# Optimization experiments

Hardware: AMD Instinct MI355X
Metric: run time of the kernel (lower is better)

Reference implementation:

```python
import jax, jax.numpy as jnp
import numpy as np

EPS = 1e-5

def layer_norm(x, w, b):
    # Faithful to the module: divides by (sqrt(var) + eps), NOT sqrt(var + eps).
    m = jnp.mean(x, axis=-1, keepdims=True)
    v = jnp.mean((x - m) ** 2, axis=-1, keepdims=True)
    return (x - m) / (jnp.sqrt(v) + EPS) * w + b

def setup_inputs() -> dict:
    key = jax.random.key(0)
    B, S, E, H, F = 8, 2048, 512, 8, 2048
    ks = jax.random.split(key, 8)
    def lin(k, fin, fout):
        k1, k2 = jax.random.split(k)
        return (jax.random.normal(k1, (fin, fout), jnp.float32) * (1.0 / np.sqrt(fin)),
                jax.random.normal(k2, (fout,), jnp.float32) * 0.01)
    WQ, bQ = lin(ks[0], E, E)
    WK, bK = lin(ks[1], E, E)
    WV, bV = lin(ks[2], E, E)
    WY, bY = lin(ks[3], E, E)
    W1, b1 = lin(ks[4], E, F)
    W2, b2 = lin(ks[5], F, E)
    x = jax.random.normal(ks[6], (B, S, E), jnp.float32)
    return {
        "x": x,
        "WQ": WQ, "bQ": bQ, "WK": WK, "bK": bK, "WV": WV, "bV": bV,
        "WY": WY, "bY": bY,
        "ln1_w": jnp.ones((E,), jnp.float32), "ln1_b": jnp.zeros((E,), jnp.float32),
        "W1": W1, "b1": b1, "W2": W2, "b2": b2,
        "ln2_w": jnp.ones((E,), jnp.float32), "ln2_b": jnp.zeros((E,), jnp.float32),
    }

def attention(x, WQ, bQ, WK, bK, WV, bV, WY, bY, num_heads=8):
    B, S, E = x.shape
    D = E // num_heads  # head_size
    def split(t):  # (B,S,E) -> (B,H,S,D)
        return t.reshape(B, S, num_heads, D).transpose(0, 2, 1, 3)
    q = split(x @ WQ + bQ)
    k = split(x @ WK + bK)
    v = split(x @ WV + bV)
    scores = jnp.einsum('bhsd,bhtd->bhst', q, k) / jnp.sqrt(jnp.float32(D))
    w = jax.nn.softmax(scores, axis=-1)  # full (B,H,S,S) attention matrix, as in original
    y = jnp.einsum('bhst,bhtd->bhsd', w, v)
    y = y.transpose(0, 2, 1, 3).reshape(B, S, E)  # merge heads
    return y @ WY + bY

def reference(x, WQ, bQ, WK, bK, WV, bV, WY, bY, ln1_w, ln1_b, W1, b1, W2, b2, ln2_w, ln2_b):
    attn_out = attention(x, WQ, bQ, WK, bK, WV, bV, WY, bY)
    h = layer_norm(x + attn_out, ln1_w, ln1_b)  # post-norm
    mlp = jax.nn.gelu(h @ W1 + b1, approximate=False) @ W2 + b2
    out = layer_norm(h + mlp, ln2_w, ln2_b)
    return out
```

## Files before the change

kernel.cpp:

```cpp
#include <hip/hip_runtime.h>
#include <hip/hip_bf16.h>
#include <cstdint>

typedef unsigned short u16;
typedef __bf16 __attribute__((ext_vector_type(8))) bf16x8;
typedef float __attribute__((ext_vector_type(4))) f32x4;
typedef float __attribute__((ext_vector_type(16))) f32x16;

#define B_ 8
#define S_ 2048
#define E_ 512
#define H_ 8
#define D_ 64
#define F_ 2048
#define MTOT (B_ * S_)
#define QSCALE 0.18033688011112042f
#define MFIX 12.0f

static __device__ __forceinline__ float bf2f(u16 u) {
    union { uint32_t i; float f; } x;
    x.i = ((uint32_t)u) << 16;
    return x.f;
}
static __device__ __forceinline__ u16 f2bf(float f) {
    __hip_bfloat16 h = __float2bfloat16(f);
    return *reinterpret_cast<u16*>(&h);
}
static __device__ __forceinline__ float fast_exp2(float x) {
    float r;
    asm("v_exp_f32 %0, %1" : "=v"(r) : "v"(x));
    return r;
}
static __device__ __forceinline__ float fast_exp2_neg(float x) {
    float r;
    asm("v_exp_f32 %0, -%1" : "=v"(r) : "v"(x));
    return r;
}
static __device__ __forceinline__ float fast_rcp(float x) {
    float r;
    asm("v_rcp_f32 %0, %1" : "=v"(r) : "v"(x));
    return r;
}
static __device__ __forceinline__ uint32_t cvt_pk_bf16(float a, float b) {
    uint32_t r;
    asm("v_cvt_pk_bf16_f32 %0, %1, %2" : "=v"(r) : "v"(a), "v"(b));
    return r;
}
static __device__ __forceinline__ float fast_gelu(float v) {
    float x2 = v * v;
    float w = v * fmaf(0.10294818f, x2, 2.3022066f);
    float e = fast_exp2_neg(w);
    return v * fast_rcp(1.0f + e);
}

__global__ __launch_bounds__(256) void prep(const float* __restrict__ x,
                                            u16* __restrict__ xb,
                                            const float* __restrict__ WQ,
                                            const float* __restrict__ WK,
                                            const float* __restrict__ WV,
                                            const float* __restrict__ WY,
                                            const float* __restrict__ W1,
                                            const float* __restrict__ W2,
                                            u16* __restrict__ WQKVT,
                                            u16* __restrict__ WYT,
                                            u16* __restrict__ W1T,
                                            u16* __restrict__ W2T,
                                            const float* __restrict__ bQ,
                                            const float* __restrict__ bK,
                                            const float* __restrict__ bV,
                                            float* __restrict__ bqkv) {
    const int bid = blockIdx.x;
    const int tid = threadIdx.x;
    if (bid < 4096) {
        int i = bid * 256 + tid;
        const float4* p = reinterpret_cast<const float4*>(x) + (size_t)i * 2;
        float4 a = p[0], b = p[1];
        uint4 o;
        o.x = cvt_pk_bf16(a.x, a.y);
        o.y = cvt_pk_bf16(a.z, a.w);
        o.z = cvt_pk_bf16(b.x, b.y);
        o.w = cvt_pk_bf16(b.z, b.w);
        *reinterpret_cast<uint4*>(xb + (size_t)i * 8) = o;
        return;
    }
    int r = bid - 4096;
    if (r >= 3072) {
        int i = (r - 3072) * 256 + tid;
        if (i < 1536) bqkv[i] = i < 512 ? bQ[i] : (i < 1024 ? bK[i - 512] : bV[i - 1024]);
        return;
    }
    __shared__ float tile[32][33];
    const float* src;
    u16* dst;
    int K, N, bx, by;
    if (r < 1024) {
        int w = r >> 8, idx = r & 255;
        bx = idx & 15; by = idx >> 4; K = 512; N = 512;
        src = w == 0 ? WQ : (w == 1 ? WK : (w == 2 ? WV : WY));
        dst = (w == 3) ? WYT : (WQKVT + (size_t)w * 512 * 512);
    } else if (r < 2048) {
        int idx = r - 1024;
        bx = idx & 63; by = idx >> 6; K = 512; N = 2048;
        src = W1; dst = W1T;
    } else {
        int idx = r - 2048;
        bx = idx & 15; by = idx >> 4; K = 2048; N = 512;
        src = W2; dst = W2T;
    }
    const int tx = tid & 31, ty = tid >> 5;
    int n0 = bx * 32, k0 = by * 32;
    for (int i = ty; i < 32; i += 8)
        tile[i][tx] = src[(size_t)(k0 + i) * N + n0 + tx];
    __syncthreads();
    for (int i = ty; i < 32; i += 8)
        dst[(size_t)(n0 + i) * K + k0 + tx] = f2bf(tile[tx][i]);
}

template <int ACT, int SPLIT>
__global__ __launch_bounds__(512) void gemm_bt(const u16* __restrict__ A,
                                               const u16* __restrict__ BT,
                                               const float* __restrict__ bias,
                                               void* __restrict__ Cv,
                                               u16* __restrict__ Vtg,
                                               int Mdim, int Ndim, int Kdim) {
    __shared__ u16 As[128 * 64];
    __shared__ u16 Bs[128 * 64];
    const int tid = threadIdx.x;
    const int wave = tid >> 6, lane = tid & 63;
    const int lr = lane & 15, lg = lane >> 4;

    const int gx = gridDim.x;
    int lin = blockIdx.y * gx + blockIdx.x;
    const int nwg = gx * gridDim.y;
    if ((nwg & 7) == 0) {
        int cpx = nwg >> 3;
        lin = (lin & 7) * cpx + (lin >> 3);
    }
    const int m0 = (lin / gx) * 128, n0 = (lin % gx) * 128;
    const int wrow = (wave >> 2) * 64, wcol = (wave & 3) * 32;

    f32x4 acc[4][2];
#pragma unroll
    for (int i = 0; i < 4; i++)
#pragma unroll
        for (int j = 0; j < 2; j++) acc[i][j] = (f32x4){0.f, 0.f, 0.f, 0.f};

    const int stagerow = tid >> 3;
    const int stagechunk = (tid & 7) * 8;

    for (int k0 = 0; k0 < Kdim; k0 += 64) {
        __syncthreads();
#pragma unroll
        for (int it = 0; it < 2; ++it) {
            int row = stagerow + it * 64;
            const u16* ga = A + (size_t)(m0 + row) * Kdim + k0 + stagechunk;
            const u16* gb = BT + (size_t)(n0 + row) * Kdim + k0 + stagechunk;
            __builtin_amdgcn_global_load_lds(
                (const __attribute__((address_space(1))) void*)ga,
                (__attribute__((address_space(3))) void*)(As + row * 64 + stagechunk),
                16, 0, 0);
            __builtin_amdgcn_global_load_lds(
                (const __attribute__((address_space(1))) void*)gb,
                (__attribute__((address_space(3))) void*)(Bs + row * 64 + stagechunk),
                16, 0, 0);
        }
        __syncthreads();
#pragma unroll
        for (int kk = 0; kk < 64; kk += 32) {
            bf16x8 af[4], bfr[2];
#pragma unroll
            for (int i = 0; i < 4; i++)
                af[i] = *reinterpret_cast<const bf16x8*>(As + (wrow + i * 16 + lr) * 64 + kk + lg * 8);
#pragma unroll
            for (int j = 0; j < 2; j++)
                bfr[j] = *reinterpret_cast<const bf16x8*>(Bs + (wcol + j * 16 + lr) * 64 + kk + lg * 8);
#pragma unroll
            for (int i = 0; i < 4; i++)
#pragma unroll
                for (int j = 0; j < 2; j++)
                    acc[i][j] = __builtin_amdgcn_mfma_f32_16x16x32_bf16(af[i], bfr[j], acc[i][j], 0, 0, 0);
        }
    }

#pragma unroll
    for (int j = 0; j < 2; j++) {
        int col = n0 + wcol + j * 16 + lr;
        float bv = bias[col];
        int seg = col >> 9, c2 = col & 511;
#pragma unroll
        for (int i = 0; i < 4; i++) {
            int rowb = m0 + wrow + i * 16 + lg * 4;
            float vv[4];
#pragma unroll
            for (int r = 0; r < 4; r++) {
                float v = acc[i][j][r] + bv;
                if (ACT == 1) v = fast_gelu(v);
                if (SPLIT) { if (seg == 0) v *= QSCALE; }
                vv[r] = v;
            }
            uint32_t p01 = cvt_pk_bf16(vv[0], vv[1]);
            uint32_t p23 = cvt_pk_bf16(vv[2], vv[3]);
            if (SPLIT) {
                if (seg == 2) {
                    int bb = rowb >> 11, s = rowb & 2047;
                    *reinterpret_cast<uint2*>(Vtg + ((size_t)bb * E_ + c2) * S_ + s) =
                        (uint2){p01, p23};
                } else {
                    u16* dst = (u16*)Cv + (size_t)seg * ((size_t)MTOT * 512) + (size_t)rowb * 512 + c2;
                    dst[0] = (u16)p01; dst[512] = (u16)(p01 >> 16);
                    dst[1024] = (u16)p23; dst[1536] = (u16)(p23 >> 16);
                }
            } else {
                u16* dst = (u16*)Cv + (size_t)rowb * Ndim + col;
                dst[0] = (u16)p01; dst[Ndim] = (u16)(p01 >> 16);
                dst[2 * (size_t)Ndim] = (u16)p23; dst[3 * (size_t)Ndim] = (u16)(p23 >> 16);
            }
        }
    }
}

__global__ __launch_bounds__(512, 4) void attn_fwd(const u16* __restrict__ Q,
                                                   const u16* __restrict__ K,
                                                   const u16* __restrict__ Vt,
                                                   u16* __restrict__ Y) {
    __shared__ u16 Ks[64 * 64];
    __shared__ u16 Vs[64 * 64];
    const int tid = threadIdx.x;
    const int wave = tid >> 6, lane = tid & 63;
    const int l31 = lane & 31, h = lane >> 5;
    const int lin = blockIdx.x;
    const int idx = lin >> 3;
    const int bh = (lin & 7) + 8 * (idx >> 3);
    const int s0 = (idx & 7) * 256;
    const int b = bh >> 3, hd = bh & 7;
    const size_t headoff = ((size_t)b * S_) * E_ + (size_t)hd * D_;
    const size_t vtoff = (size_t)bh * D_ * S_;
    const int qb = s0 + wave * 32;
    const int sw31 = l31 & 7;

    bf16x8 qf[4];
    {
        const u16* qrow = Q + headoff + (size_t)(qb + l31) * E_ + h * 8;
#pragma unroll
        for (int db = 0; db < 4; db++)
            qf[db] = *reinterpret_cast<const bf16x8*>(qrow + db * 16);
    }
    f32x16 o0 = {0.f, 0.f, 0.f, 0.f, 0.f, 0.f, 0.f, 0.f,
                 0.f, 0.f, 0.f, 0.f, 0.f, 0.f, 0.f, 0.f};
    f32x16 o1 = o0;
    float lrow = 0.f;

    const int r8 = lane >> 3, c8 = lane & 7;
    const int srcch = c8 ^ r8;
    const int strow = wave * 8 + r8;

    auto STAGE_K = [&](int t) {
        const u16* gk = K + headoff + (size_t)(t * 64 + strow) * E_ + srcch * 8;
        __builtin_amdgcn_global_load_lds(
            (const __attribute__((address_space(1))) void*)gk,
            (__attribute__((address_space(3))) void*)(Ks + strow * 64 + c8 * 8), 16, 0, 0);
    };
    auto STAGE_V = [&](int t) {
        const u16* gv = Vt + vtoff + (size_t)strow * S_ + t * 64 + srcch * 8;
        __builtin_amdgcn_global_load_lds(
            (const __attribute__((address_space(1))) void*)gv,
            (__attribute__((address_space(3))) void*)(Vs + strow * 64 + c8 * 8), 16, 0, 0);
    };

    STAGE_K(0);
    STAGE_V(0);
    __syncthreads();

    for (int t = 0; t < S_ / 64; ++t) {
        f32x16 sc0 = {-MFIX, -MFIX, -MFIX, -MFIX, -MFIX, -MFIX, -MFIX, -MFIX,
                      -MFIX, -MFIX, -MFIX, -MFIX, -MFIX, -MFIX, -MFIX, -MFIX};
        f32x16 sc1 = sc0;
        __builtin_amdgcn_s_setprio(1);
#pragma unroll
        for (int db = 0; db < 4; db++) {
            int cc = ((db * 2 + h) ^ sw31) * 8;
            bf16x8 a0 = *reinterpret_cast<const bf16x8*>(Ks + l31 * 64 + cc);
            bf16x8 a1 = *reinterpret_cast<const bf16x8*>(Ks + (32 + l31) * 64 + cc);
            sc0 = __builtin_amdgcn_mfma_f32_32x32x16_bf16(a0, qf[db], sc0, 0, 0, 0);
            sc1 = __builtin_amdgcn_mfma_f32_32x32x16_bf16(a1, qf[db], sc1, 0, 0, 0);
        }
        __builtin_amdgcn_s_setprio(0);
        __syncthreads();
        if (t + 1 < S_ / 64) STAGE_K(t + 1);

        bf16x8 pa[4];
        float rs = 0.f;
#pragma unroll
        for (int kh = 0; kh < 2; kh++) {
#pragma unroll
            for (int f = 0; f < 2; f++) {
                float p0, p1, p2, p3, p4, p5, p6, p7;
                if (kh == 0) {
                    if (f == 0) {
                        p0 = fast_exp2(sc0[0]); p1 = fast_exp2(sc0[1]);
                        p2 = fast_exp2(sc0[2]); p3 = fast_exp2(sc0[3]);
                        p4 = fast_exp2(sc0[4]); p5 = fast_exp2(sc0[5]);
                        p6 = fast_exp2(sc0[6]); p7 = fast_exp2(sc0[7]);
                    } else {
                        p0 = fast_exp2(sc0[8]);  p1 = fast_exp2(sc0[9]);
                        p2 = fast_exp2(sc0[10]); p3 = fast_exp2(sc0[11]);
                        p4 = fast_exp2(sc0[12]); p5 = fast_exp2(sc0[13]);
                        p6 = fast_exp2(sc0[14]); p7 = fast_exp2(sc0[15]);
                    }
                } else {
                    if (f == 0) {
                        p0 = fast_exp2(sc1[0]); p1 = fast_exp2(sc1[1]);
                        p2 = fast_exp2(sc1[2]); p3 = fast_exp2(sc1[3]);
                        p4 = fast_exp2(sc1[4]); p5 = fast_exp2(sc1[5]);
                        p6 = fast_exp2(sc1[6]); p7 = fast_exp2(sc1[7]);
                    } else {
                        p0 = fast_exp2(sc1[8]);  p1 = fast_exp2(sc1[9]);
                        p2 = fast_exp2(sc1[10]); p3 = fast_exp2(sc1[11]);
                        p4 = fast_exp2(sc1[12]); p5 = fast_exp2(sc1[13]);
                        p6 = fast_exp2(sc1[14]); p7 = fast_exp2(sc1[15]);
                    }
                }
                rs += ((p0 + p1) + (p2 + p3)) + ((p4 + p5) + (p6 + p7));
                uint32_t x0 = cvt_pk_bf16(p0, p1);
                uint32_t x1 = cvt_pk_bf16(p2, p3);
                uint32_t y0 = cvt_pk_bf16(p4, p5);
                uint32_t y1 = cvt_pk_bf16(p6, p7);
                asm("v_permlane32_swap_b32 %0, %1" : "+v"(x0), "+v"(y0));
                asm("v_permlane32_swap_b32 %0, %1" : "+v"(x1), "+v"(y1));
                uint4 av = {x0, x1, y0, y1};
                pa[kh * 2 + f] = *reinterpret_cast<const bf16x8*>(&av);
            }
        }
        rs += __shfl_xor(rs, 32);
        lrow += rs;

        __builtin_amdgcn_s_setprio(1);
#pragma unroll
        for (int s = 0; s < 4; s++) {
            int cc = ((s * 2 + h) ^ sw31) * 8;
            bf16x8 bv0 = *reinterpret_cast<const bf16x8*>(Vs + l31 * 64 + cc);
            bf16x8 bv1 = *reinterpret_cast<const bf16x8*>(Vs + (32 + l31) * 64 + cc);
            o0 = __builtin_amdgcn_mfma_f32_32x32x16_bf16(pa[s], bv0, o0, 0, 0, 0);
            o1 = __builtin_amdgcn_mfma_f32_32x32x16_bf16(pa[s], bv1, o1, 0, 0, 0);
        }
        __builtin_amdgcn_s_setprio(0);
        __syncthreads();
        if (t + 1 < S_ / 64) STAGE_V(t + 1);
    }

#pragma unroll
    for (int r = 0; r < 16; r++) {
        int q = (r & 3) + 8 * (r >> 2) + 4 * h;
        float rl = fast_rcp(__shfl(lrow, q));
        u16* dst = Y + headoff + (size_t)(qb + q) * E_ + l31;
        dst[0] = f2bf(o0[r] * rl);
        dst[32] = f2bf(o1[r] * rl);
    }
}

template <int F32OUT>
__global__ __launch_bounds__(256) void resid_ln(const u16* __restrict__ X,
                                                const u16* __restrict__ Yres,
                                                const float* __restrict__ W,
                                                const float* __restrict__ Bb,
                                                void* __restrict__ H) {
    const int tid = threadIdx.x;
    const int wave = tid >> 6, lane = tid & 63;
    const size_t row = (size_t)blockIdx.x * 4 + wave;
    uint4 xa = *reinterpret_cast<const uint4*>(X + row * E_ + lane * 8);
    uint4 ya = *reinterpret_cast<const uint4*>(Yres + row * E_ + lane * 8);
    const u16* xu = reinterpret_cast<const u16*>(&xa);
    const u16* yu = reinterpret_cast<const u16*>(&ya);
    float v[8];
    float s = 0.f, sq = 0.f;
#pragma unroll
    for (int e = 0; e < 8; e++) {
        v[e] = bf2f(xu[e]) + bf2f(yu[e]);
        s += v[e];
        sq += v[e] * v[e];
    }
#pragma unroll
    for (int msk = 1; msk < 64; msk <<= 1) {
        s += __shfl_xor(s, msk);
        sq += __shfl_xor(sq, msk);
    }
    float mean = s * (1.f / E_);
    float var = fmaxf(sq * (1.f / E_) - mean * mean, 0.f);
    float rstd = 1.f / (sqrtf(var) + 1e-5f);
    const float4* wr = reinterpret_cast<const float4*>(W + lane * 8);
    const float4* br = reinterpret_cast<const float4*>(Bb + lane * 8);
    float4 w0 = wr[0], w1 = wr[1], b0 = br[0], b1 = br[1];
    float wv[8] = {w0.x, w0.y, w0.z, w0.w, w1.x, w1.y, w1.z, w1.w};
    float bv[8] = {b0.x, b0.y, b0.z, b0.w, b1.x, b1.y, b1.z, b1.w};
    float out[8];
#pragma unroll
    for (int e = 0; e < 8; e++) out[e] = (v[e] - mean) * rstd * wv[e] + bv[e];
    if (F32OUT) {
        float4* hw = reinterpret_cast<float4*>((float*)H + row * E_ + lane * 8);
        hw[0] = (float4){out[0], out[1], out[2], out[3]};
        hw[1] = (float4){out[4], out[5], out[6], out[7]};
    } else {
        uint4 ob;
        ob.x = cvt_pk_bf16(out[0], out[1]);
        ob.y = cvt_pk_bf16(out[2], out[3]);
        ob.z = cvt_pk_bf16(out[4], out[5]);
        ob.w = cvt_pk_bf16(out[6], out[7]);
        *reinterpret_cast<uint4*>((u16*)H + row * E_ + lane * 8) = ob;
    }
}

extern "C" void kernel_launch(void* const* d_in, const int* in_sizes, int n_in,
                              void* d_out, int out_size, void* d_ws, size_t ws_size,
                              hipStream_t stream) {
    const float* x = (const float*)d_in[0];
    const float* WQ = (const float*)d_in[1];
    const float* bQ = (const float*)d_in[2];
    const float* WK = (const float*)d_in[3];
    const float* bK = (const float*)d_in[4];
    const float* WV = (const float*)d_in[5];
    const float* bV = (const float*)d_in[6];
    const float* WY = (const float*)d_in[7];
    const float* bY = (const float*)d_in[8];
    const float* ln1w = (const float*)d_in[9];
    const float* ln1b = (const float*)d_in[10];
    const float* W1 = (const float*)d_in[11];
    const float* b1 = (const float*)d_in[12];
    const float* W2 = (const float*)d_in[13];
    const float* b2 = (const float*)d_in[14];
    const float* ln2w = (const float*)d_in[15];
    const float* ln2b = (const float*)d_in[16];

    char* ws = (char*)d_ws;
    const size_t MB = 1024 * 1024;
    u16* WQKVT = (u16*)(ws);
    u16* WYT = (u16*)(ws + (size_t)1536 * 1024);
    u16* W1T = (u16*)(ws + 2 * MB);
    u16* W2T = (u16*)(ws + 4 * MB);
    float* bqkv = (float*)(ws + 6 * MB);
    u16* xb   = (u16*)(ws + 7 * MB);
    u16* Qb   = (u16*)(ws + 23 * MB);
    u16* Kb   = (u16*)(ws + 39 * MB);
    u16* Vtg  = (u16*)(ws + 55 * MB);
    u16* Yb   = (u16*)(ws + 71 * MB);
    u16* attnb = Vtg;
    u16* hb   = Qb;
    u16* hid  = Kb;
    u16* m2b  = xb;

    dim3 blk(256);
    dim3 gblk(512);
    prep<<<dim3(7174), blk, 0, stream>>>(x, xb, WQ, WK, WV, WY, W1, W2,
                                         WQKVT, WYT, W1T, W2T, bQ, bK, bV, bqkv);
    gemm_bt<0, 1><<<dim3(12, 128), gblk, 0, stream>>>(xb, WQKVT, bqkv, Qb, Vtg, MTOT, 1536, 512);
    attn_fwd<<<dim3(512), dim3(512), 0, stream>>>(Qb, Kb, Vtg, Yb);
    gemm_bt<0, 0><<<dim3(4, 128), gblk, 0, stream>>>(Yb, WYT, bY, attnb, nullptr, MTOT, 512, 512);
    resid_ln<0><<<dim3(4096), blk, 0, stream>>>(xb, attnb, ln1w, ln1b, hb);
    gemm_bt<1, 0><<<dim3(16, 128), gblk, 0, stream>>>(hb, W1T, b1, hid, nullptr, MTOT, 2048, 512);
    gemm_bt<0, 0><<<dim3(4, 128), gblk, 0, stream>>>(hid, W2T, b2, m2b, nullptr, MTOT, 512, 2048);
    resid_ln<1><<<dim3(4096), blk, 0, stream>>>(hb, m2b, ln2w, ln2b, (float*)d_out);
}
```

Before: 277.6 us.

## Process two query groups per wave in attention to reuse K/V LDS fragments

The attention kernel now uses 4 waves of 256 threads instead of 8 waves of 512. Each wave handles 64 query rows as two 32-row groups, so every K and V fragment read from LDS feeds two MFMAs instead of one. Each thread stages two rows per K/V tile to keep the 64-row tile fill. This halves LDS fragment reads per MFMA and block-wide barrier participants, but doubles accumulator and score registers per wave and lowers waves per block, which may reduce latency hiding.

```diff
diff --git a/kernel.cpp b/kernel.cpp
--- a/kernel.cpp
+++ b/kernel.cpp
@@ -219,7 +219,7 @@
     }
 }
 
-__global__ __launch_bounds__(512, 4) void attn_fwd(const u16* __restrict__ Q,
+__global__ __launch_bounds__(256, 2) void attn_fwd(const u16* __restrict__ Q,
                                                    const u16* __restrict__ K,
                                                    const u16* __restrict__ Vt,
                                                    u16* __restrict__ Y) {
@@ -235,36 +235,48 @@
     const int b = bh >> 3, hd = bh & 7;
     const size_t headoff = ((size_t)b * S_) * E_ + (size_t)hd * D_;
     const size_t vtoff = (size_t)bh * D_ * S_;
-    const int qb = s0 + wave * 32;
+    const int qb = s0 + wave * 64;
     const int sw31 = l31 & 7;
 
-    bf16x8 qf[4];
-    {
-        const u16* qrow = Q + headoff + (size_t)(qb + l31) * E_ + h * 8;
+    bf16x8 qf[2][4];
+#pragma unroll
+    for (int qg = 0; qg < 2; qg++) {
+        const u16* qrow = Q + headoff + (size_t)(qb + qg * 32 + l31) * E_ + h * 8;
 #pragma unroll
         for (int db = 0; db < 4; db++)
-            qf[db] = *reinterpret_cast<const bf16x8*>(qrow + db * 16);
-    }
-    f32x16 o0 = {0.f, 0.f, 0.f, 0.f, 0.f, 0.f, 0.f, 0.f,
-                 0.f, 0.f, 0.f, 0.f, 0.f, 0.f, 0.f, 0.f};
-    f32x16 o1 = o0;
-    float lrow = 0.f;
+            qf[qg][db] = *reinterpret_cast<const bf16x8*>(qrow + db * 16);
+    }
+    f32x16 o[2][2];
+#pragma unroll
+    for (int qg = 0; qg < 2; qg++)
+#pragma unroll
+        for (int dh = 0; dh < 2; dh++)
+#pragma unroll
+            for (int e = 0; e < 16; e++) o[qg][dh][e] = 0.f;
+    float lrow[2] = {0.f, 0.f};
 
     const int r8 = lane >> 3, c8 = lane & 7;
     const int srcch = c8 ^ r8;
-    const int strow = wave * 8 + r8;
 
     auto STAGE_K = [&](int t) {
-        const u16* gk = K + headoff + (size_t)(t * 64 + strow) * E_ + srcch * 8;
-        __builtin_amdgcn_global_load_lds(
-            (const __attribute__((address_space(1))) void*)gk,
-            (__attribute__((address_space(3))) void*)(Ks + strow * 64 + c8 * 8), 16, 0, 0);
+#pragma unroll
+        for (int it = 0; it < 2; ++it) {
+            int row = wave * 8 + it * 32 + r8;
+            const u16* gk = K + headoff + (size_t)(t * 64 + row) * E_ + srcch * 8;
+            __builtin_amdgcn_global_load_lds(
+                (const __attribute__((address_space(1))) void*)gk,
+                (__attribute__((address_space(3))) void*)(Ks + row * 64 + c8 * 8), 16, 0, 0);
+        }
     };
     auto STAGE_V = [&](int t) {
-        const u16* gv = Vt + vtoff + (size_t)strow * S_ + t * 64 + srcch * 8;
-        __builtin_amdgcn_global_load_lds(
-            (const __attribute__((address_space(1))) void*)gv,
-            (__attribute__((address_space(3))) void*)(Vs + strow * 64 + c8 * 8), 16, 0, 0);
+#pragma unroll
+        for (int it = 0; it < 2; ++it) {
+            int row = wave * 8 + it * 32 + r8;
+            const u16* gv = Vt + vtoff + (size_t)row * S_ + t * 64 + srcch * 8;
+            __builtin_amdgcn_global_load_lds(
+                (const __attribute__((address_space(1))) void*)gv,
+                (__attribute__((address_space(3))) void*)(Vs + row * 64 + c8 * 8), 16, 0, 0);
+        }
     };
 
     STAGE_K(0);
@@ -272,67 +284,55 @@
     __syncthreads();
 
     for (int t = 0; t < S_ / 64; ++t) {
-        f32x16 sc0 = {-MFIX, -MFIX, -MFIX, -MFIX, -MFIX, -MFIX, -MFIX, -MFIX,
-                      -MFIX, -MFIX, -MFIX, -MFIX, -MFIX, -MFIX, -MFIX, -MFIX};
-        f32x16 sc1 = sc0;
+        f32x16 sc[2][2];
+#pragma unroll
+        for (int qg = 0; qg < 2; qg++)
+#pragma unroll
+            for (int kh = 0; kh < 2; kh++)
+#pragma unroll
+                for (int e = 0; e < 16; e++) sc[qg][kh][e] = -MFIX;
         __builtin_amdgcn_s_setprio(1);
 #pragma unroll
         for (int db = 0; db < 4; db++) {
             int cc = ((db * 2 + h) ^ sw31) * 8;
             bf16x8 a0 = *reinterpret_cast<const bf16x8*>(Ks + l31 * 64 + cc);
             bf16x8 a1 = *reinterpret_cast<const bf16x8*>(Ks + (32 + l31) * 64 + cc);
-            sc0 = __builtin_amdgcn_mfma_f32_32x32x16_bf16(a0, qf[db], sc0, 0, 0, 0);
-            sc1 = __builtin_amdgcn_mfma_f32_32x32x16_bf16(a1, qf[db], sc1, 0, 0, 0);
+#pragma unroll
+            for (int qg = 0; qg < 2; qg++) {
+                sc[qg][0] = __builtin_amdgcn_mfma_f32_32x32x16_bf16(a0, qf[qg][db], sc[qg][0], 0, 0, 0);
+                sc[qg][1] = __builtin_amdgcn_mfma_f32_32x32x16_bf16(a1, qf[qg][db], sc[qg][1], 0, 0, 0);
+            }
         }
         __builtin_amdgcn_s_setprio(0);
         __syncthreads();
         if (t + 1 < S_ / 64) STAGE_K(t + 1);
 
-        bf16x8 pa[4];
-        float rs = 0.f;
-#pragma unroll
-        for (int kh = 0; kh < 2; kh++) {
-#pragma unroll
-            for (int f = 0; f < 2; f++) {
-                float p0, p1, p2, p3, p4, p5, p6, p7;
-                if (kh == 0) {
-                    if (f == 0) {
-                        p0 = fast_exp2(sc0[0]); p1 = fast_exp2(sc0[1]);
-                        p2 = fast_exp2(sc0[2]); p3 = fast_exp2(sc0[3]);
-                        p4 = fast_exp2(sc0[4]); p5 = fast_exp2(sc0[5]);
-                        p6 = fast_exp2(sc0[6]); p7 = fast_exp2(sc0[7]);
-                    } else {
-                        p0 = fast_exp2(sc0[8]);  p1 = fast_exp2(sc0[9]);
-                        p2 = fast_exp2(sc0[10]); p3 = fast_exp2(sc0[11]);
-                        p4 = fast_exp2(sc0[12]); p5 = fast_exp2(sc0[13]);
-                        p6 = fast_exp2(sc0[14]); p7 = fast_exp2(sc0[15]);
-                    }
-                } else {
-                    if (f == 0) {
-                        p0 = fast_exp2(sc1[0]); p1 = fast_exp2(sc1[1]);
-                        p2 = fast_exp2(sc1[2]); p3 = fast_exp2(sc1[3]);
-                        p4 = fast_exp2(sc1[4]); p5 = fast_exp2(sc1[5]);
-                        p6 = fast_exp2(sc1[6]); p7 = fast_exp2(sc1[7]);
-                    } else {
-                        p0 = fast_exp2(sc1[8]);  p1 = fast_exp2(sc1[9]);
-                        p2 = fast_exp2(sc1[10]); p3 = fast_exp2(sc1[11]);
-                        p4 = fast_exp2(sc1[12]); p5 = fast_exp2(sc1[13]);
-                        p6 = fast_exp2(sc1[14]); p7 = fast_exp2(sc1[15]);
-                    }
+        bf16x8 paa[2][4];
+#pragma unroll
+        for (int qg = 0; qg < 2; qg++) {
+            float rs = 0.f;
+#pragma unroll
+            for (int kh = 0; kh < 2; kh++) {
+#pragma unroll
+                for (int f = 0; f < 2; f++) {
+                    float p[8];
+#pragma unroll
+                    for (int e = 0; e < 8; e++)
+                        p[e] = fast_exp2(sc[qg][kh][f * 8 + e]);
+                    rs += ((p[0] + p[1]) + (p[2] + p[3])) + ((p[4] + p[5]) + (p[6] + p[7]));
+                    uint32_t x0 = cvt_pk_bf16(p[0], p[1]);
+                    uint32_t x1 = cvt_pk_bf16(p[2], p[3]);
+                    uint32_t y0 = cvt_pk_bf16(p[4], p[5]);
+                    uint32_t y1 = cvt_pk_bf16(p[6], p[7]);
+                    asm("v_permlane32_swap_b32 %0, %1" : "+v"(x0), "+v"(y0));
+                    asm("v_permlane32_swap_b32 %0, %1" : "+v"(x1), "+v"(y1));
+                    uint4 av = {x0, x1, y0, y1};
+                    paa[qg][kh * 2 + f] = *reinterpret_cast<const bf16x8*>(&av);
                 }
-                rs += ((p0 + p1) + (p2 + p3)) + ((p4 + p5) + (p6 + p7));
-                uint32_t x0 = cvt_pk_bf16(p0, p1);
-                uint32_t x1 = cvt_pk_bf16(p2, p3);
-                uint32_t y0 = cvt_pk_bf16(p4, p5);
-                uint32_t y1 = cvt_pk_bf16(p6, p7);
-                asm("v_permlane32_swap_b32 %0, %1" : "+v"(x0), "+v"(y0));
-                asm("v_permlane32_swap_b32 %0, %1" : "+v"(x1), "+v"(y1));
-                uint4 av = {x0, x1, y0, y1};
-                pa[kh * 2 + f] = *reinterpret_cast<const bf16x8*>(&av);
             }
-        }
-        rs += __shfl_xor(rs, 32);
-        lrow += rs;
+            rs += __shfl_xor(rs, 32);
+            lrow[qg] += rs;
+        }
 
         __builtin_amdgcn_s_setprio(1);
 #pragma unroll
@@ -340,8 +340,11 @@
             int cc = ((s * 2 + h) ^ sw31) * 8;
             bf16x8 bv0 = *reinterpret_cast<const bf16x8*>(Vs + l31 * 64 + cc);
             bf16x8 bv1 = *reinterpret_cast<const bf16x8*>(Vs + (32 + l31) * 64 + cc);
-            o0 = __builtin_amdgcn_mfma_f32_32x32x16_bf16(pa[s], bv0, o0, 0, 0, 0);
-            o1 = __builtin_amdgcn_mfma_f32_32x32x16_bf16(pa[s], bv1, o1, 0, 0, 0);
+#pragma unroll
+            for (int qg = 0; qg < 2; qg++) {
+                o[qg][0] = __builtin_amdgcn_mfma_f32_32x32x16_bf16(paa[qg][s], bv0, o[qg][0], 0, 0, 0);
+                o[qg][1] = __builtin_amdgcn_mfma_f32_32x32x16_bf16(paa[qg][s], bv1, o[qg][1], 0, 0, 0);
+            }
         }
         __builtin_amdgcn_s_setprio(0);
         __syncthreads();
@@ -349,12 +352,15 @@
     }
 
 #pragma unroll
-    for (int r = 0; r < 16; r++) {
-        int q = (r & 3) + 8 * (r >> 2) + 4 * h;
-        float rl = fast_rcp(__shfl(lrow, q));
-        u16* dst = Y + headoff + (size_t)(qb + q) * E_ + l31;
-        dst[0] = f2bf(o0[r] * rl);
-        dst[32] = f2bf(o1[r] * rl);
+    for (int qg = 0; qg < 2; qg++) {
+#pragma unroll
+        for (int r = 0; r < 16; r++) {
+            int q = (r & 3) + 8 * (r >> 2) + 4 * h;
+            float rl = fast_rcp(__shfl(lrow[qg], q));
+            u16* dst = Y + headoff + (size_t)(qb + qg * 32 + q) * E_ + l31;
+            dst[0] = f2bf(o[qg][0][r] * rl);
+            dst[32] = f2bf(o[qg][1][r] * rl);
+        }
     }
 }
 
@@ -452,7 +458,7 @@
     prep<<<dim3(7174), blk, 0, stream>>>(x, xb, WQ, WK, WV, WY, W1, W2,
                                          WQKVT, WYT, W1T, W2T, bQ, bK, bV, bqkv);
     gemm_bt<0, 1><<<dim3(12, 128), gblk, 0, stream>>>(xb, WQKVT, bqkv, Qb, Vtg, MTOT, 1536, 512);
-    attn_fwd<<<dim3(512), dim3(512), 0, stream>>>(Qb, Kb, Vtg, Yb);
+    attn_fwd<<<dim3(512), blk, 0, stream>>>(Qb, Kb, Vtg, Yb);
     gemm_bt<0, 0><<<dim3(4, 128), gblk, 0, stream>>>(Yb, WYT, bY, attnb, nullptr, MTOT, 512, 512);
     resid_ln<0><<<dim3(4096), blk, 0, stream>>>(xb, attnb, ln1w, ln1b, hb);
     gemm_bt<1, 0><<<dim3(16, 128), gblk, 0, stream>>>(hb, W1T, b1, hid, nullptr, MTOT, 2048, 512);
```

After: 280.8 us. About the same (+1.2%).
